# Optimization experiments

Hardware: AMD Instinct MI355X
Metric: run time of the kernel (lower is better)

Reference implementation:

```python
import jax, jax.numpy as jnp
import numpy as np

NUM_CAMS = 4
E = 256          # embed_dim
H_HEADS = 8      # num_heads
DH = E // H_HEADS
CIN = 64
FF = 4 * E
N_LAYERS = 2
EPS = 1e-5


def _layer_norm(x, g, b):
    mu = jnp.mean(x, axis=-1, keepdims=True)
    var = jnp.mean((x - mu) ** 2, axis=-1, keepdims=True)
    return (x - mu) * jax.lax.rsqrt(var + EPS) * g + b


def setup_inputs() -> dict:
    key = jax.random.key(0)
    ks = jax.random.split(key, 20)
    s = 0.02
    inp = {
        "features": jax.random.normal(ks[0], (NUM_CAMS, 2, CIN, 96, 96), jnp.float32),
        # 1x1 input projection conv
        "Wp": jax.random.normal(ks[1], (E, CIN), jnp.float32) * s,
        "bp": jnp.zeros((E,), jnp.float32),
        # per-layer attention params (stacked over 2 layers)
        "Wqkv": jax.random.normal(ks[2], (N_LAYERS, 3 * E, E), jnp.float32) * s,
        "bqkv": jnp.zeros((N_LAYERS, 3 * E), jnp.float32),
        "Wo": jax.random.normal(ks[3], (N_LAYERS, E, E), jnp.float32) * s,
        "bo": jnp.zeros((N_LAYERS, E), jnp.float32),
        # FFN
        "W1": jax.random.normal(ks[4], (N_LAYERS, FF, E), jnp.float32) * s,
        "b1": jnp.zeros((N_LAYERS, FF), jnp.float32),
        "W2": jax.random.normal(ks[5], (N_LAYERS, E, FF), jnp.float32) * s,
        "b2": jnp.zeros((N_LAYERS, E), jnp.float32),
        # LayerNorms
        "g1": jnp.ones((N_LAYERS, E), jnp.float32),
        "be1": jnp.zeros((N_LAYERS, E), jnp.float32),
        "g2": jnp.ones((N_LAYERS, E), jnp.float32),
        "be2": jnp.zeros((N_LAYERS, E), jnp.float32),
        # 1x1 output conv
        "Wout": jax.random.normal(ks[6], (CIN, E), jnp.float32) * s,
        "bout": jnp.zeros((CIN,), jnp.float32),
    }
    return inp


def reference(features, Wp, bp, Wqkv, bqkv, Wo, bo, W1, b1, W2, b2,
              g1, be1, g2, be2, Wout, bout):
    n_cam, B, Cin, Hh, Ww = features.shape
    # 1x1 conv projection + rearrange to per-pixel sequences: [B*H*W, n_cam, E]
    x = jnp.einsum('nbchw,ec->bhwne', features, Wp) + bp
    x = x.reshape(B * Hh * Ww, n_cam, E)

    scale = 1.0 / jnp.sqrt(jnp.float32(DH))
    for i in range(N_LAYERS):
        # self-attention (post-norm encoder layer, dropout=identity in eval)
        qkv = x @ Wqkv[i].T + bqkv[i]                      # [N, S, 3E]
        q, k, v = jnp.split(qkv, 3, axis=-1)
        q = q.reshape(-1, n_cam, H_HEADS, DH)
        k = k.reshape(-1, n_cam, H_HEADS, DH)
        v = v.reshape(-1, n_cam, H_HEADS, DH)
        scores = jnp.einsum('nqhd,nkhd->nhqk', q, k) * scale
        attn = jax.nn.softmax(scores, axis=-1)
        sa = jnp.einsum('nhqk,nkhd->nqhd', attn, v).reshape(-1, n_cam, E)
        sa = sa @ Wo[i].T + bo[i]
        x = _layer_norm(x + sa, g1[i], be1[i])
        # FFN (ReLU activation, default)
        ff = jax.nn.relu(x @ W1[i].T + b1[i]) @ W2[i].T + b2[i]
        x = _layer_norm(x + ff, g2[i], be2[i])

    # mean over cameras, back to [B, C, H, W] via 1x1 output conv
    fused = x.mean(axis=1).reshape(B, Hh, Ww, E)
    out = jnp.einsum('bhwe,ce->bchw', fused, Wout) + bout[None, :, None, None]
    return out
```

## Files before the change

### kernel.cpp

```cpp
#include <hip/hip_runtime.h>
#include <cstdint>
#include <cstddef>


typedef __bf16 bf16;
typedef __bf16 bf16x8 __attribute__((ext_vector_type(8)));
typedef __bf16 bf16x4 __attribute__((ext_vector_type(4)));
typedef float  f32x4  __attribute__((ext_vector_type(4)));

__device__ __forceinline__ void async_copy16(const void* g, void* l)
{
    __builtin_amdgcn_global_load_lds(
        (__attribute__((address_space(1))) void*)g,
        (__attribute__((address_space(3))) void*)l,
        16, 0, 0);
}

#define WAITV8_BAR() asm volatile("s_waitcnt vmcnt(8)\ns_barrier" ::: "memory")
#define WAITV4_BAR() asm volatile("s_waitcnt vmcnt(4)\ns_barrier" ::: "memory")
#define WAITV0_BAR() asm volatile("s_waitcnt vmcnt(0)\ns_barrier" ::: "memory")
#define WAITL_BAR()  asm volatile("s_waitcnt lgkmcnt(0)\ns_barrier" ::: "memory")

__global__ void pack_all_k(const float* __restrict__ s0, const float* __restrict__ s1,
                           const float* __restrict__ s2, const float* __restrict__ s3,
                           const float* __restrict__ s4,
                           bf16* __restrict__ d0, bf16* __restrict__ d1,
                           bf16* __restrict__ d2, bf16* __restrict__ d3,
                           bf16* __restrict__ d4)
{
    const int i = blockIdx.x * 256 + threadIdx.x;
    if (i < 393216)       d0[i] = (bf16)s0[i];
    else if (i < 524288)  d1[i - 393216] = (bf16)s1[i - 393216];
    else if (i < 1048576) d2[i - 524288] = (bf16)s2[i - 524288];
    else if (i < 1572864) d3[i - 1048576] = (bf16)s3[i - 1048576];
    else                  d4[i - 1572864] = (bf16)s4[i - 1572864];
}

__global__ __launch_bounds__(256) void feat_pack_k(const float* __restrict__ feat,
                                                   bf16* __restrict__ Xf)
{
    __shared__ float ft[64][68];

    const int tid  = threadIdx.x;
    const int camb = blockIdx.y;
    const int cam  = camb >> 1;
    const int b    = camb & 1;
    const int hw0  = blockIdx.x * 64;

    const float* fb = feat + (size_t)camb * 64 * 9216 + hw0;
#pragma unroll
    for (int rep = 0; rep < 16; ++rep) {
        const int idx = rep * 256 + tid;
        const int c = idx >> 6, p = idx & 63;
        ft[p][c] = fb[(size_t)c * 9216 + p];
    }
    __syncthreads();

    const int pbase = b * 9216 + hw0;
#pragma unroll
    for (int rep = 0; rep < 2; ++rep) {
        const int idx = rep * 256 + tid;
        const int p = idx >> 3, cc = idx & 7;
        const f32x4 a = *(const f32x4*)(&ft[p][cc * 8]);
        const f32x4 c4 = *(const f32x4*)(&ft[p][cc * 8 + 4]);
        bf16x8 v;
#pragma unroll
        for (int i = 0; i < 4; ++i) { v[i] = (bf16)a[i]; v[4 + i] = (bf16)c4[i]; }
        const size_t t = (size_t)(pbase + p) * 4 + cam;
        *(bf16x8*)(Xf + t * 64 + cc * 8) = v;
    }
}

template <bool RELU>
__global__ __launch_bounds__(256, 2) void gemm_bt(
    const bf16* __restrict__ A, const bf16* __restrict__ B,
    const float* __restrict__ bias, bf16* __restrict__ C,
    int N, int K)
{
    __shared__ __align__(16) char smem[65536];

    const int tid  = threadIdx.x;
    const int lane = tid & 63;
    const int wv   = tid >> 6;
    const int wm   = wv >> 1;
    const int wn   = wv & 1;
    const int bm   = blockIdx.y * 128;
    const int bn   = blockIdx.x * 128;

    const int r8  = lane >> 3;
    const int p8  = lane & 7;
    const int gch = p8 ^ r8;

    const int quad = lane >> 4;
    const int l16  = lane & 15;

    f32x4 acc[4][4] = {};
    const int nk = K >> 6;

    auto STAGE = [&](int kc, char* base) {
#pragma unroll
        for (int inst = 0; inst < 4; ++inst) {
            const int row = wv * 32 + inst * 8 + r8;
            async_copy16(A + (size_t)(bm + row) * K + (kc * 64 + gch * 8),
                         base + (wv * 4 + inst) * 1024);
            async_copy16(B + (size_t)(bn + row) * K + (kc * 64 + gch * 8),
                         base + 16384 + (wv * 4 + inst) * 1024);
        }
    };

    STAGE(0, smem);

#pragma unroll 1
    for (int kc = 0; kc < nk; ++kc) {
        const char* cur = smem + (size_t)(kc & 1) * 32768;
        if (kc + 1 < nk) {
            STAGE(kc + 1, smem + (size_t)((kc + 1) & 1) * 32768);
            WAITV8_BAR();
        } else {
            WAITV0_BAR();
        }

#pragma unroll
        for (int kk = 0; kk < 2; ++kk) {
            bf16x8 af[4], bfr[4];
            const int lch = kk * 4 + quad;
#pragma unroll
            for (int i = 0; i < 4; ++i) {
                const int m = wm * 64 + i * 16 + l16;
                af[i] = *(const bf16x8*)(cur + (m * 8 + (lch ^ (m & 7))) * 16);
                const int n = wn * 64 + i * 16 + l16;
                bfr[i] = *(const bf16x8*)(cur + 16384 + (n * 8 + (lch ^ (n & 7))) * 16);
            }
            __builtin_amdgcn_s_setprio(1);
#pragma unroll
            for (int i = 0; i < 4; ++i)
#pragma unroll
                for (int j = 0; j < 4; ++j)
                    acc[i][j] = __builtin_amdgcn_mfma_f32_16x16x32_bf16(
                        af[i], bfr[j], acc[i][j], 0, 0, 0);
            __builtin_amdgcn_s_setprio(0);
        }
        WAITL_BAR();
    }

#pragma unroll
    for (int j = 0; j < 4; ++j) {
        const int n = bn + wn * 64 + j * 16 + l16;
        const float bv = bias[n];
#pragma unroll
        for (int i = 0; i < 4; ++i) {
            const int mb = bm + wm * 64 + i * 16 + quad * 4;
#pragma unroll
            for (int r = 0; r < 4; ++r) {
                float v = acc[i][j][r] + bv;
                if (RELU) v = fmaxf(v, 0.f);
                C[(size_t)(mb + r) * N + n] = (bf16)v;
            }
        }
    }
}

__device__ __forceinline__ void wo_stage(const bf16* __restrict__ Wo, int kc,
                                         char* buf, int tid)
{
#pragma unroll
    for (int it = 0; it < 4; ++it) {
        const int L = it * 256 + tid;
        const int r128 = L >> 3, psl = L & 7;
        const int g = psl ^ (r128 & 7);
        const int n = r128 * 2 + (g >> 2);
        const int c = g & 3;
        async_copy16(Wo + (size_t)n * 256 + kc * 32 + c * 8,
                     buf + (size_t)L * 16);
    }
}

__global__ __launch_bounds__(256, 2) void attn_ln_k(
    const bf16* __restrict__ QKV, const bf16* __restrict__ Wo,
    const float* __restrict__ bias, const bf16* __restrict__ Xres,
    const float* __restrict__ gam, const float* __restrict__ bet,
    bf16* __restrict__ Xout)
{
    __shared__ __align__(16) char smem[66560];
    bf16* SAs  = (bf16*)smem;
    char* Bbuf = smem + 32768;
    float2 (*red)[2] = (float2 (*)[2])(void*)(smem + 65536);

    const int tid  = threadIdx.x;
    const int lane = tid & 63;
    const int wv   = tid >> 6;
    const int wm   = wv >> 1;
    const int wn   = wv & 1;
    const int quad = lane >> 4;
    const int l16  = lane & 15;
    const int bm   = blockIdx.x * 64;

    wo_stage(Wo, 0, Bbuf, tid);

    {
        const int hh = lane >> 3;
        const int cg = lane & 7;
        const int s0 = blockIdx.x * 16;
        const float SCALE = 0.17677669529663687f;

#pragma unroll
        for (int g = 0; g < 4; ++g) {
            const int seq = s0 + g * 4 + wv;
            const bf16* bse = QKV + (size_t)seq * 3072 + hh * 32 + cg * 4;

            float qf[4][4], kf[4][4], vf[4][4];
#pragma unroll
            for (int i = 0; i < 4; ++i) {
                const bf16x4 qb = *(const bf16x4*)(bse + i * 768);
                const bf16x4 kb = *(const bf16x4*)(bse + i * 768 + 256);
                const bf16x4 vb = *(const bf16x4*)(bse + i * 768 + 512);
#pragma unroll
                for (int d = 0; d < 4; ++d) {
                    qf[i][d] = (float)qb[d];
                    kf[i][d] = (float)kb[d];
                    vf[i][d] = (float)vb[d];
                }
            }

            float sc[4][4];
#pragma unroll
            for (int i = 0; i < 4; ++i)
#pragma unroll
                for (int j = 0; j < 4; ++j)
                    sc[i][j] = qf[i][0] * kf[j][0] + qf[i][1] * kf[j][1]
                             + qf[i][2] * kf[j][2] + qf[i][3] * kf[j][3];

#pragma unroll
            for (int msk = 1; msk <= 4; msk <<= 1)
#pragma unroll
                for (int i = 0; i < 4; ++i)
#pragma unroll
                    for (int j = 0; j < 4; ++j)
                        sc[i][j] += __shfl_xor(sc[i][j], msk, 64);

#pragma unroll
            for (int i = 0; i < 4; ++i) {
                const float v0 = sc[i][0] * SCALE, v1 = sc[i][1] * SCALE;
                const float v2 = sc[i][2] * SCALE, v3 = sc[i][3] * SCALE;
                const float mx = fmaxf(fmaxf(v0, v1), fmaxf(v2, v3));
                const float e0 = expf(v0 - mx), e1 = expf(v1 - mx);
                const float e2 = expf(v2 - mx), e3 = expf(v3 - mx);
                const float inv = 1.f / (e0 + e1 + e2 + e3);
                sc[i][0] = e0 * inv; sc[i][1] = e1 * inv;
                sc[i][2] = e2 * inv; sc[i][3] = e3 * inv;
            }

#pragma unroll
            for (int i = 0; i < 4; ++i) {
                bf16x4 ov;
#pragma unroll
                for (int d = 0; d < 4; ++d) {
                    const float o = sc[i][0] * vf[0][d] + sc[i][1] * vf[1][d]
                                  + sc[i][2] * vf[2][d] + sc[i][3] * vf[3][d];
                    ov[d] = (bf16)o;
                }
                const int m  = (g * 4 + wv) * 4 + i;
                const int gc = lane >> 1;
                const int sl = (gc & 24) | ((gc ^ m) & 7);
                *(bf16x4*)((char*)SAs + (m * 32 + sl) * 16 + (lane & 1) * 8) = ov;
            }
        }
    }
    __syncthreads();

    f32x4 acc[2][8] = {};

#pragma unroll
    for (int s = 0; s < 8; ++s) {
        const char* cur = Bbuf + (size_t)(s & 1) * 16384;
        if (s < 7) {
            wo_stage(Wo, s + 1, Bbuf + (size_t)((s + 1) & 1) * 16384, tid);
            WAITV4_BAR();
        } else {
            WAITV0_BAR();
        }
        const int gc = s * 4 + quad;
        bf16x8 af[2], bfr[8];
#pragma unroll
        for (int i = 0; i < 2; ++i) {
            const int m  = wm * 32 + i * 16 + l16;
            const int sl = (gc & 24) | ((gc ^ m) & 7);
            af[i] = *(const bf16x8*)((const char*)SAs + (m * 32 + sl) * 16);
        }
#pragma unroll
        for (int j = 0; j < 8; ++j) {
            const int n  = wn * 128 + j * 16 + l16;
            const int sl = (((n & 1) * 4 + quad) ^ ((n >> 1) & 7)) & 7;
            bfr[j] = *(const bf16x8*)(cur + ((n >> 1) * 8 + sl) * 16);
        }
        __builtin_amdgcn_s_setprio(1);
#pragma unroll
        for (int i = 0; i < 2; ++i)
#pragma unroll
            for (int j = 0; j < 8; ++j)
                acc[i][j] = __builtin_amdgcn_mfma_f32_16x16x32_bf16(
                    af[i], bfr[j], acc[i][j], 0, 0, 0);
        __builtin_amdgcn_s_setprio(0);
        WAITL_BAR();
    }

    float bv[8], gv[8], bev[8];
#pragma unroll
    for (int j = 0; j < 8; ++j) {
        const int n = wn * 128 + j * 16 + l16;
        bv[j] = bias[n]; gv[j] = gam[n]; bev[j] = bet[n];
    }

#pragma unroll
    for (int i = 0; i < 2; ++i) {
#pragma unroll
        for (int r = 0; r < 4; ++r) {
            const int rl = wm * 32 + i * 16 + quad * 4 + r;
            const size_t row = (size_t)(bm + rl);
            float s1 = 0.f, s2 = 0.f;
#pragma unroll
            for (int j = 0; j < 8; ++j) {
                const int n = wn * 128 + j * 16 + l16;
                const float v = acc[i][j][r] + bv[j] + (float)Xres[row * 256 + n];
                acc[i][j][r] = v;
                s1 += v; s2 += v * v;
            }
#pragma unroll
            for (int off = 1; off < 16; off <<= 1) {
                s1 += __shfl_xor(s1, off, 64);
                s2 += __shfl_xor(s2, off, 64);
            }
            if (l16 == 0) red[rl][wn] = make_float2(s1, s2);
        }
    }
    __syncthreads();

#pragma unroll
    for (int i = 0; i < 2; ++i) {
#pragma unroll
        for (int r = 0; r < 4; ++r) {
            const int rl = wm * 32 + i * 16 + quad * 4 + r;
            const float2 p0 = red[rl][0], p1 = red[rl][1];
            const float mu  = (p0.x + p1.x) * (1.f / 256.f);
            const float ex2 = (p0.y + p1.y) * (1.f / 256.f);
            const float rstd = rsqrtf(fmaxf(ex2 - mu * mu, 0.f) + 1e-5f);
            const size_t row = (size_t)(bm + rl);
#pragma unroll
            for (int j = 0; j < 8; ++j) {
                const int n = wn * 128 + j * 16 + l16;
                Xout[row * 256 + n] = (bf16)((acc[i][j][r] - mu) * rstd * gv[j] + bev[j]);
            }
        }
    }
}

__device__ __forceinline__ void ffn_stage(int s, int rot, const bf16* __restrict__ W1,
                                          const bf16* __restrict__ W2,
                                          char* buf, int tid)
{
    const int hc = ((s >> 3) + rot) & 7;
    const int q  = s & 7;
    if (q < 4) {
#pragma unroll
        for (int it = 0; it < 4; ++it) {
            const int L = it * 256 + tid;
            const int row = L >> 3, psl = L & 7;
            const int c = psl ^ (row & 7);
            async_copy16(W1 + (size_t)(hc * 128 + row) * 256 + q * 64 + c * 8,
                         buf + (size_t)L * 16);
        }
    } else {
#pragma unroll
        for (int it = 0; it < 4; ++it) {
            const int L = it * 256 + tid;
            const int r128 = L >> 3, psl = L & 7;
            const int g = psl ^ (r128 & 7);
            const int n = r128 * 2 + (g >> 2);
            const int c = g & 3;
            async_copy16(W2 + (size_t)n * 1024 + hc * 128 + (q - 4) * 32 + c * 8,
                         buf + (size_t)L * 16);
        }
    }
}

__global__ __launch_bounds__(256, 2) void ffn_fused_k(
    const bf16* __restrict__ X,
    const bf16* __restrict__ W1, const float* __restrict__ b1,
    const bf16* __restrict__ W2, const float* __restrict__ b2,
    const float* __restrict__ gam, const float* __restrict__ bet,
    bf16* __restrict__ Xout)
{
    __shared__ __align__(16) char smem[81920];
    bf16* Xs = (bf16*)smem;
    bf16* Ts = (bf16*)(smem + 32768);
    float2 (*red)[2] = (float2 (*)[2])(void*)(smem + 32768);
    char* stg = smem + 49152;

    const int tid  = threadIdx.x;
    const int lane = tid & 63;
    const int wv   = tid >> 6;
    const int wm   = wv >> 1;
    const int wn   = wv & 1;
    const int quad = lane >> 4;
    const int l16  = lane & 15;
    const int bm   = blockIdx.x * 64;
    const int rot  = (blockIdx.x >> 3) & 7;

#pragma unroll
    for (int it = 0; it < 8; ++it) {
        const int L = it * 256 + tid;
        const int row = L >> 5, slot = L & 31;
        const int gch = (slot & 24) | ((slot ^ row) & 7);
        async_copy16(X + (size_t)(bm + row) * 256 + gch * 8,
                     (char*)Xs + (size_t)L * 16);
    }
    ffn_stage(0, rot, W1, W2, stg, tid);
    ffn_stage(1, rot, W1, W2, stg + 16384, tid);

    f32x4 acc2[2][8] = {};

#pragma unroll 1
    for (int hc = 0; hc < 8; ++hc) {
        const int hcr = (hc + rot) & 7;
        float b1v[4];
#pragma unroll
        for (int j = 0; j < 4; ++j)
            b1v[j] = b1[hcr * 128 + wn * 64 + j * 16 + l16];

        f32x4 accA[2][4] = {};

#pragma unroll
        for (int q = 0; q < 4; ++q) {
            const int s = hc * 8 + q;
            const char* cur = stg + (size_t)(q & 1) * 16384;
            ffn_stage(s + 1, rot, W1, W2, stg + (size_t)((q + 1) & 1) * 16384, tid);
            WAITV4_BAR();
#pragma unroll
            for (int kk = 0; kk < 2; ++kk) {
                const int ch = kk * 4 + quad;
                const int gc = q * 8 + ch;
                bf16x8 af[2], bfr[4];
#pragma unroll
                for (int i = 0; i < 2; ++i) {
                    const int m  = wm * 32 + i * 16 + l16;
                    const int sl = (gc & 24) | ((gc ^ m) & 7);
                    af[i] = *(const bf16x8*)((const char*)Xs + (m * 32 + sl) * 16);
                }
#pragma unroll
                for (int j = 0; j < 4; ++j) {
                    const int n  = wn * 64 + j * 16 + l16;
                    const int sl = ch ^ (n & 7);
                    bfr[j] = *(const bf16x8*)(cur + (n * 8 + sl) * 16);
                }
                __builtin_amdgcn_s_setprio(1);
#pragma unroll
                for (int i = 0; i < 2; ++i)
#pragma unroll
                    for (int j = 0; j < 4; ++j)
                        accA[i][j] = __builtin_amdgcn_mfma_f32_16x16x32_bf16(
                            af[i], bfr[j], accA[i][j], 0, 0, 0);
                __builtin_amdgcn_s_setprio(0);
            }
            WAITL_BAR();
        }

#pragma unroll
        for (int j = 0; j < 4; ++j) {
            const int h  = wn * 64 + j * 16 + l16;
            const float bb = b1v[j];
            const int g  = h >> 3;
#pragma unroll
            for (int i = 0; i < 2; ++i)
#pragma unroll
                for (int r = 0; r < 4; ++r) {
                    const int m  = wm * 32 + i * 16 + quad * 4 + r;
                    const int sl = (g & 8) | ((g ^ m) & 7);
                    const float v = fmaxf(accA[i][j][r] + bb, 0.f);
                    *((bf16*)((char*)Ts + (m * 16 + sl) * 16 + (h & 7) * 2)) = (bf16)v;
                }
        }
        WAITL_BAR();

#pragma unroll
        for (int q = 0; q < 4; ++q) {
            const int s = hc * 8 + 4 + q;
            const char* cur = stg + (size_t)(q & 1) * 16384;
            if (s < 63) {
                ffn_stage(s + 1, rot, W1, W2, stg + (size_t)((q + 1) & 1) * 16384, tid);
                WAITV4_BAR();
            } else {
                WAITV0_BAR();
            }
            const int tc = q * 4 + quad;
            bf16x8 af[2], bfr[8];
#pragma unroll
            for (int i = 0; i < 2; ++i) {
                const int m  = wm * 32 + i * 16 + l16;
                const int sl = (tc & 8) | ((tc ^ m) & 7);
                af[i] = *(const bf16x8*)((const char*)Ts + (m * 16 + sl) * 16);
            }
#pragma unroll
            for (int j = 0; j < 8; ++j) {
                const int n  = wn * 128 + j * 16 + l16;
                const int sl = (((n & 1) * 4 + quad) ^ ((n >> 1) & 7)) & 7;
                bfr[j] = *(const bf16x8*)(cur + ((n >> 1) * 8 + sl) * 16);
            }
            __builtin_amdgcn_s_setprio(1);
#pragma unroll
            for (int i = 0; i < 2; ++i)
#pragma unroll
                for (int j = 0; j < 8; ++j)
                    acc2[i][j] = __builtin_amdgcn_mfma_f32_16x16x32_bf16(
                        af[i], bfr[j], acc2[i][j], 0, 0, 0);
            __builtin_amdgcn_s_setprio(0);
            WAITL_BAR();
        }
    }

    float bv[8], gv[8], bev[8];
#pragma unroll
    for (int j = 0; j < 8; ++j) {
        const int n = wn * 128 + j * 16 + l16;
        bv[j] = b2[n]; gv[j] = gam[n]; bev[j] = bet[n];
    }

#pragma unroll
    for (int i = 0; i < 2; ++i) {
#pragma unroll
        for (int r = 0; r < 4; ++r) {
            const int rl = wm * 32 + i * 16 + quad * 4 + r;
            float s1 = 0.f, s2 = 0.f;
#pragma unroll
            for (int j = 0; j < 8; ++j) {
                const int n  = wn * 128 + j * 16 + l16;
                const int gc = n >> 3;
                const int sl = (gc & 24) | ((gc ^ rl) & 7);
                const float xr = (float)*((const bf16*)((const char*)Xs +
                                   (rl * 32 + sl) * 16 + (n & 7) * 2));
                const float v = acc2[i][j][r] + bv[j] + xr;
                acc2[i][j][r] = v;
                s1 += v; s2 += v * v;
            }
#pragma unroll
            for (int off = 1; off < 16; off <<= 1) {
                s1 += __shfl_xor(s1, off, 64);
                s2 += __shfl_xor(s2, off, 64);
            }
            if (l16 == 0) red[rl][wn] = make_float2(s1, s2);
        }
    }
    __syncthreads();

#pragma unroll
    for (int i = 0; i < 2; ++i) {
#pragma unroll
        for (int r = 0; r < 4; ++r) {
            const int rl = wm * 32 + i * 16 + quad * 4 + r;
            const float2 p0 = red[rl][0], p1 = red[rl][1];
            const float mu  = (p0.x + p1.x) * (1.f / 256.f);
            const float ex2 = (p0.y + p1.y) * (1.f / 256.f);
            const float rstd = rsqrtf(fmaxf(ex2 - mu * mu, 0.f) + 1e-5f);
            const size_t row = (size_t)(bm + rl);
#pragma unroll
            for (int j = 0; j < 8; ++j) {
                const int n = wn * 128 + j * 16 + l16;
                Xout[row * 256 + n] = (bf16)((acc2[i][j][r] - mu) * rstd * gv[j] + bev[j]);
            }
        }
    }
}

__global__ __launch_bounds__(256) void out_proj_k(const bf16* __restrict__ X,
                                                  const float* __restrict__ Wout,
                                                  const float* __restrict__ bout,
                                                  float* __restrict__ out)
{
    __shared__ float fused[16][260];
    const int tid = threadIdx.x;
    const int p0  = blockIdx.x * 16;

#pragma unroll
    for (int it = 0; it < 16; ++it) {
        const int idx = it * 256 + tid;
        const int pix = idx >> 8, e = idx & 255;
        const size_t base = (size_t)(p0 + pix) * 1024 + e;
        const float s = (float)X[base] + (float)X[base + 256] +
                        (float)X[base + 512] + (float)X[base + 768];
        fused[pix][e] = s * 0.25f;
    }
    __syncthreads();

    const int pix = tid & 15;
    const int c0  = tid >> 4;
    const int p   = p0 + pix;
    const int b   = p / 9216;
    const int hw  = p % 9216;
#pragma unroll
    for (int it = 0; it < 4; ++it) {
        const int c = it * 16 + c0;
        const float* w = Wout + c * 256;
        float acc = bout[c];
#pragma unroll 8
        for (int e = 0; e < 256; ++e) acc += fused[pix][e] * w[e];
        out[((size_t)b * 64 + c) * 9216 + hw] = acc;
    }
}

extern "C" void kernel_launch(void* const* d_in, const int* in_sizes, int n_in,
                              void* d_out, int out_size, void* d_ws, size_t ws_size,
                              hipStream_t stream)
{
    const float* features = (const float*)d_in[0];
    const float* Wp   = (const float*)d_in[1];
    const float* bp   = (const float*)d_in[2];
    const float* Wqkv = (const float*)d_in[3];
    const float* bqkv = (const float*)d_in[4];
    const float* Wo   = (const float*)d_in[5];
    const float* bo   = (const float*)d_in[6];
    const float* W1   = (const float*)d_in[7];
    const float* b1   = (const float*)d_in[8];
    const float* W2   = (const float*)d_in[9];
    const float* b2   = (const float*)d_in[10];
    const float* g1   = (const float*)d_in[11];
    const float* be1  = (const float*)d_in[12];
    const float* g2   = (const float*)d_in[13];
    const float* be2  = (const float*)d_in[14];
    const float* Wout = (const float*)d_in[15];
    const float* bout = (const float*)d_in[16];
    float* out = (float*)d_out;

    char* ws = (char*)d_ws;
    bf16* X   = (bf16*)(ws);
    bf16* QKV = (bf16*)(ws + 37748736ull);
    bf16* Xf  = (bf16*)(ws + 188743680ull);
    bf16* WpB = (bf16*)(ws + 198180864ull);
    bf16* Wb  = (bf16*)(ws + 226492416ull);

    bf16* WqkvB = Wb;
    bf16* WoB   = Wb + 393216;
    bf16* W1B   = Wb + 524288;
    bf16* W2B   = Wb + 1048576;

    pack_all_k<<<6208, 256, 0, stream>>>(Wqkv, Wo, W1, W2, Wp,
                                         WqkvB, WoB, W1B, W2B, WpB);

    feat_pack_k<<<dim3(144, 8), 256, 0, stream>>>(features, Xf);
    gemm_bt<false><<<dim3(2, 576), 256, 0, stream>>>(Xf, WpB, bp, X, 256, 64);

    for (int l = 0; l < 2; ++l) {
        gemm_bt<false><<<dim3(6, 576), 256, 0, stream>>>(
            X, WqkvB + l * 196608, bqkv + l * 768, QKV, 768, 256);
        attn_ln_k<<<1152, 256, 0, stream>>>(
            QKV, WoB + l * 65536, bo + l * 256, X,
            g1 + l * 256, be1 + l * 256, X);
        ffn_fused_k<<<1152, 256, 0, stream>>>(
            X, W1B + l * 262144, b1 + l * 1024,
            W2B + l * 262144, b2 + l * 256,
            g2 + l * 256, be2 + l * 256, X);
    }

    out_proj_k<<<1152, 256, 0, stream>>>(X, Wout, bout, out);
}
```

Measured before the change: 603.2 us.

## Load weight fragments directly from global memory instead of LDS staging

Removes the double-buffered async LDS staging of Wo, W1 and W2 in the attention and FFN kernels. Each wave now loads its MFMA B fragments straight from global memory (relying on L2/L1 caching), with a per-block rotation added in the attention kernel to spread accesses. This cuts LDS footprint and per-step barriers, which may allow higher occupancy. In exchange it issues redundant global loads across waves and exposes load latency without explicit prefetch.

```diff
diff --git a/kernel.cpp b/kernel.cpp
--- a/kernel.cpp
+++ b/kernel.cpp
@@ -17,7 +17,6 @@
 }
 
 #define WAITV8_BAR() asm volatile("s_waitcnt vmcnt(8)\ns_barrier" ::: "memory")
-#define WAITV4_BAR() asm volatile("s_waitcnt vmcnt(4)\ns_barrier" ::: "memory")
 #define WAITV0_BAR() asm volatile("s_waitcnt vmcnt(0)\ns_barrier" ::: "memory")
 #define WAITL_BAR()  asm volatile("s_waitcnt lgkmcnt(0)\ns_barrier" ::: "memory")
 
@@ -160,31 +159,15 @@
     }
 }
 
-__device__ __forceinline__ void wo_stage(const bf16* __restrict__ Wo, int kc,
-                                         char* buf, int tid)
-{
-#pragma unroll
-    for (int it = 0; it < 4; ++it) {
-        const int L = it * 256 + tid;
-        const int r128 = L >> 3, psl = L & 7;
-        const int g = psl ^ (r128 & 7);
-        const int n = r128 * 2 + (g >> 2);
-        const int c = g & 3;
-        async_copy16(Wo + (size_t)n * 256 + kc * 32 + c * 8,
-                     buf + (size_t)L * 16);
-    }
-}
-
 __global__ __launch_bounds__(256, 2) void attn_ln_k(
     const bf16* __restrict__ QKV, const bf16* __restrict__ Wo,
     const float* __restrict__ bias, const bf16* __restrict__ Xres,
     const float* __restrict__ gam, const float* __restrict__ bet,
     bf16* __restrict__ Xout)
 {
-    __shared__ __align__(16) char smem[66560];
-    bf16* SAs  = (bf16*)smem;
-    char* Bbuf = smem + 32768;
-    float2 (*red)[2] = (float2 (*)[2])(void*)(smem + 65536);
+    __shared__ __align__(16) char smem[33792];
+    bf16* SAs = (bf16*)smem;
+    float2 (*red)[2] = (float2 (*)[2])(void*)(smem + 32768);
 
     const int tid  = threadIdx.x;
     const int lane = tid & 63;
@@ -194,8 +177,7 @@
     const int quad = lane >> 4;
     const int l16  = lane & 15;
     const int bm   = blockIdx.x * 64;
-
-    wo_stage(Wo, 0, Bbuf, tid);
+    const int rot  = (blockIdx.x >> 3) & 7;
 
     {
         const int hh = lane >> 3;
@@ -272,27 +254,20 @@
 
 #pragma unroll
     for (int s = 0; s < 8; ++s) {
-        const char* cur = Bbuf + (size_t)(s & 1) * 16384;
-        if (s < 7) {
-            wo_stage(Wo, s + 1, Bbuf + (size_t)((s + 1) & 1) * 16384, tid);
-            WAITV4_BAR();
-        } else {
-            WAITV0_BAR();
-        }
-        const int gc = s * 4 + quad;
+        const int sr = (s + rot) & 7;
+        const int gc = sr * 4 + quad;
         bf16x8 af[2], bfr[8];
+#pragma unroll
+        for (int j = 0; j < 8; ++j) {
+            const int n = wn * 128 + j * 16 + l16;
+            bfr[j] = *(const bf16x8*)(Wo + (size_t)n * 256 + sr * 32 + quad * 8);
+        }
 #pragma unroll
         for (int i = 0; i < 2; ++i) {
             const int m  = wm * 32 + i * 16 + l16;
             const int sl = (gc & 24) | ((gc ^ m) & 7);
             af[i] = *(const bf16x8*)((const char*)SAs + (m * 32 + sl) * 16);
         }
-#pragma unroll
-        for (int j = 0; j < 8; ++j) {
-            const int n  = wn * 128 + j * 16 + l16;
-            const int sl = (((n & 1) * 4 + quad) ^ ((n >> 1) & 7)) & 7;
-            bfr[j] = *(const bf16x8*)(cur + ((n >> 1) * 8 + sl) * 16);
-        }
         __builtin_amdgcn_s_setprio(1);
 #pragma unroll
         for (int i = 0; i < 2; ++i)
@@ -301,7 +276,6 @@
                 acc[i][j] = __builtin_amdgcn_mfma_f32_16x16x32_bf16(
                     af[i], bfr[j], acc[i][j], 0, 0, 0);
         __builtin_amdgcn_s_setprio(0);
-        WAITL_BAR();
     }
 
     float bv[8], gv[8], bev[8];
@@ -354,35 +328,6 @@
     }
 }
 
-__device__ __forceinline__ void ffn_stage(int s, int rot, const bf16* __restrict__ W1,
-                                          const bf16* __restrict__ W2,
-                                          char* buf, int tid)
-{
-    const int hc = ((s >> 3) + rot) & 7;
-    const int q  = s & 7;
-    if (q < 4) {
-#pragma unroll
-        for (int it = 0; it < 4; ++it) {
-            const int L = it * 256 + tid;
-            const int row = L >> 3, psl = L & 7;
-            const int c = psl ^ (row & 7);
-            async_copy16(W1 + (size_t)(hc * 128 + row) * 256 + q * 64 + c * 8,
-                         buf + (size_t)L * 16);
-        }
-    } else {
-#pragma unroll
-        for (int it = 0; it < 4; ++it) {
-            const int L = it * 256 + tid;
-            const int r128 = L >> 3, psl = L & 7;
-            const int g = psl ^ (r128 & 7);
-            const int n = r128 * 2 + (g >> 2);
-            const int c = g & 3;
-            async_copy16(W2 + (size_t)n * 1024 + hc * 128 + (q - 4) * 32 + c * 8,
-                         buf + (size_t)L * 16);
-        }
-    }
-}
-
 __global__ __launch_bounds__(256, 2) void ffn_fused_k(
     const bf16* __restrict__ X,
     const bf16* __restrict__ W1, const float* __restrict__ b1,
@@ -390,11 +335,10 @@
     const float* __restrict__ gam, const float* __restrict__ bet,
     bf16* __restrict__ Xout)
 {
-    __shared__ __align__(16) char smem[81920];
+    __shared__ __align__(16) char smem[49152];
     bf16* Xs = (bf16*)smem;
     bf16* Ts = (bf16*)(smem + 32768);
     float2 (*red)[2] = (float2 (*)[2])(void*)(smem + 32768);
-    char* stg = smem + 49152;
 
     const int tid  = threadIdx.x;
     const int lane = tid & 63;
@@ -414,14 +358,14 @@
         async_copy16(X + (size_t)(bm + row) * 256 + gch * 8,
                      (char*)Xs + (size_t)L * 16);
     }
-    ffn_stage(0, rot, W1, W2, stg, tid);
-    ffn_stage(1, rot, W1, W2, stg + 16384, tid);
+    WAITV0_BAR();
 
     f32x4 acc2[2][8] = {};
 
 #pragma unroll 1
     for (int hc = 0; hc < 8; ++hc) {
         const int hcr = (hc + rot) & 7;
+        const bf16* W1c = W1 + (size_t)hcr * 128 * 256;
         float b1v[4];
 #pragma unroll
         for (int j = 0; j < 4; ++j)
@@ -431,27 +375,22 @@
 
 #pragma unroll
         for (int q = 0; q < 4; ++q) {
-            const int s = hc * 8 + q;
-            const char* cur = stg + (size_t)(q & 1) * 16384;
-            ffn_stage(s + 1, rot, W1, W2, stg + (size_t)((q + 1) & 1) * 16384, tid);
-            WAITV4_BAR();
 #pragma unroll
             for (int kk = 0; kk < 2; ++kk) {
                 const int ch = kk * 4 + quad;
                 const int gc = q * 8 + ch;
                 bf16x8 af[2], bfr[4];
+#pragma unroll
+                for (int j = 0; j < 4; ++j) {
+                    const int n = wn * 64 + j * 16 + l16;
+                    bfr[j] = *(const bf16x8*)(W1c + (size_t)n * 256 + q * 64 + ch * 8);
+                }
 #pragma unroll
                 for (int i = 0; i < 2; ++i) {
                     const int m  = wm * 32 + i * 16 + l16;
                     const int sl = (gc & 24) | ((gc ^ m) & 7);
                     af[i] = *(const bf16x8*)((const char*)Xs + (m * 32 + sl) * 16);
                 }
-#pragma unroll
-                for (int j = 0; j < 4; ++j) {
-                    const int n  = wn * 64 + j * 16 + l16;
-                    const int sl = ch ^ (n & 7);
-                    bfr[j] = *(const bf16x8*)(cur + (n * 8 + sl) * 16);
-                }
                 __builtin_amdgcn_s_setprio(1);
 #pragma unroll
                 for (int i = 0; i < 2; ++i)
@@ -461,7 +400,6 @@
                             af[i], bfr[j], accA[i][j], 0, 0, 0);
                 __builtin_amdgcn_s_setprio(0);
             }
-            WAITL_BAR();
         }
 
 #pragma unroll
@@ -483,28 +421,20 @@
 
 #pragma unroll
         for (int q = 0; q < 4; ++q) {
-            const int s = hc * 8 + 4 + q;
-            const char* cur = stg + (size_t)(q & 1) * 16384;
-            if (s < 63) {
-                ffn_stage(s + 1, rot, W1, W2, stg + (size_t)((q + 1) & 1) * 16384, tid);
-                WAITV4_BAR();
-            } else {
-                WAITV0_BAR();
-            }
             const int tc = q * 4 + quad;
             bf16x8 af[2], bfr[8];
+#pragma unroll
+            for (int j = 0; j < 8; ++j) {
+                const int n = wn * 128 + j * 16 + l16;
+                bfr[j] = *(const bf16x8*)(W2 + (size_t)n * 1024 + hcr * 128
+                                          + q * 32 + quad * 8);
+            }
 #pragma unroll
             for (int i = 0; i < 2; ++i) {
                 const int m  = wm * 32 + i * 16 + l16;
                 const int sl = (tc & 8) | ((tc ^ m) & 7);
                 af[i] = *(const bf16x8*)((const char*)Ts + (m * 16 + sl) * 16);
             }
-#pragma unroll
-            for (int j = 0; j < 8; ++j) {
-                const int n  = wn * 128 + j * 16 + l16;
-                const int sl = (((n & 1) * 4 + quad) ^ ((n >> 1) & 7)) & 7;
-                bfr[j] = *(const bf16x8*)(cur + ((n >> 1) * 8 + sl) * 16);
-            }
             __builtin_amdgcn_s_setprio(1);
 #pragma unroll
             for (int i = 0; i < 2; ++i)
@@ -513,8 +443,8 @@
                     acc2[i][j] = __builtin_amdgcn_mfma_f32_16x16x32_bf16(
                         af[i], bfr[j], acc2[i][j], 0, 0, 0);
             __builtin_amdgcn_s_setprio(0);
-            WAITL_BAR();
-        }
+        }
+        WAITL_BAR();
     }
 
     float bv[8], gv[8], bev[8];
```

Measured after the change: 994.7 us. +64.9%, slower.
